# Optimization experiments

Measured on AMD Instinct MI355X. Metric: run time of the kernel, lower is better.

Reference implementation:

```python
import jax, jax.numpy as jnp
import numpy as np

S0, P0 = 4096, 64      # level0 segments, points per level0 segment
S1, P1 = 1024, 256     # level1 superpoints, points per level1 segment
C = 128                # feature dim
KNN = 3                # K (neighbor_range=1 -> 3 candidates)
N = S0 * P0


def setup_inputs() -> dict:
    key = jax.random.key(0)
    ks = jax.random.split(key, 8)
    return {
        "sp_center_feat": jax.random.normal(ks[0], (S1, C), jnp.float32),
        "sp_center_coord": jax.random.normal(ks[1], (S1, 3), jnp.float32),
        "rawPoint_feat": jax.random.normal(ks[2], (N, C), jnp.float32),
        "hilbert_feat_coord": jax.random.normal(ks[3], (N, 3), jnp.float32),
        "points_feat": jax.random.normal(ks[4], (S0, P0, C), jnp.float32),
        "points_coord": jax.random.normal(ks[5], (S0, P0, 3), jnp.float32),
        "level0_to_level1_indices": jnp.sort(jax.random.randint(ks[6], (S0,), 0, S1)).astype(jnp.int64),
        "num_segments0": S0,
        "points_per_segment0": P0,
        "num_segments1": S1,
        "points_per_segment1": P1,
        "K": KNN,
    }


def reference(sp_center_feat, sp_center_coord, rawPoint_feat, hilbert_feat_coord,
              points_feat, points_coord, level0_to_level1_indices,
              num_segments0, points_per_segment0, num_segments1, points_per_segment1, K):
    # --- neighbor superpoint candidates (neighbor_range = 1) ---
    offsets = jnp.arange(-1, 2)                                        # [3]
    nb = jnp.clip(jnp.arange(num_segments0)[:, None] + offsets[None, :], 0, num_segments0 - 1)  # [S0,3]
    sp_idx = level0_to_level1_indices[nb]                              # [S0,3]
    nb_feat = sp_center_feat[sp_idx]                                   # [S0,3,C]
    nb_coord = sp_center_coord[sp_idx]                                 # [S0,3,3]

    # --- cdist + topk (smallest K) ---
    diff = points_coord[:, :, None, :] - nb_coord[:, None, :, :]       # [S0,P0,3,3]
    dist = jnp.sqrt(jnp.maximum(jnp.sum(diff * diff, axis=-1), 0.0))   # [S0,P0,3]
    _, knn_idx = jax.lax.top_k(-dist, K)                               # [S0,P0,K], ascending distance

    # --- gather neighbor feats, dot-product similarity, softmax, argmax ---
    b = jnp.arange(num_segments0)[:, None, None]
    knn_sp_feats = nb_feat[b, knn_idx]                                 # [S0,P0,K,C]
    sim = jnp.einsum('spc,spkc->spk', points_feat, knn_sp_feats)       # [S0,P0,K]
    sim = jax.nn.softmax(sim, axis=-1)
    max_idx = jnp.argmax(sim, axis=-1)                                 # [S0,P0]

    # --- map winning neighbor slot -> superpoint id ---
    sp_knn = sp_idx[b, knn_idx]                                        # [S0,P0,K]
    assigned = jnp.take_along_axis(sp_knn, max_idx[..., None], axis=2)[..., 0]  # [S0,P0]
    point_assignments = assigned.reshape(-1)                           # [N]

    # cross_attention_update_sp is empty -> sp_center_feat passes through unchanged

    # --- scatter-mean: new superpoint centers ---
    seg_sum = jax.ops.segment_sum(hilbert_feat_coord, point_assignments, num_segments=num_segments1)
    counts = jax.ops.segment_sum(jnp.ones((point_assignments.shape[0],), hilbert_feat_coord.dtype),
                                 point_assignments, num_segments=num_segments1)
    new_sp_center_coord = seg_sum / jnp.maximum(counts, 1.0)[:, None]  # [S1,3]

    feat_dim = rawPoint_feat.shape[-1]
    hilbert_feat_level1 = rawPoint_feat.reshape(num_segments1, points_per_segment1, feat_dim)
    points_feat_out = rawPoint_feat.reshape(num_segments0, points_per_segment0, feat_dim)

    return (point_assignments, sp_center_feat, new_sp_center_coord, points_feat_out, hilbert_feat_level1)
```

## Files before the change

kernel.cpp:

```cpp
#include <hip/hip_runtime.h>

#define S0 4096
#define P0 64
#define S1 1024
#define P1 256
#define C  128
#define N_PTS (S0 * P0)

__global__ __launch_bounds__(256) void assign_kernel(
    const float* __restrict__ sp_feat,
    const float* __restrict__ pts_feat,
    const float* __restrict__ hilb,
    const int*   __restrict__ l01,
    float* __restrict__ out_assign,
    float* __restrict__ ws_sum,
    float* __restrict__ ws_cnt)
{
    __shared__ float cf[3][C];
    __shared__ float lsum[3][3];
    __shared__ float lcnt[3];
    __shared__ int   lidx[3];

    const int s    = blockIdx.x;
    const int tid  = threadIdx.x;
    const int wave = tid >> 6;
    const int lane = tid & 63;

    if (tid == 0) {
        int sm = (s - 1 < 0) ? 0 : s - 1;
        int sp = (s + 1 >= S0) ? S0 - 1 : s + 1;
        lidx[0] = l01[sm];
        lidx[1] = l01[s];
        lidx[2] = l01[sp];
    }
    if (tid < 9) lsum[tid / 3][tid % 3] = 0.0f;
    if (tid < 3) lcnt[tid] = 0.0f;
    __syncthreads();

    for (int i = tid; i < 3 * C; i += 256) {
        int k = i / C, c = i % C;
        cf[k][c] = sp_feat[(size_t)lidx[k] * C + c];
    }
    __syncthreads();

    const float* base = pts_feat + (size_t)s * P0 * C;
    const int c0 = lane * 2;

    for (int p = wave * 16; p < wave * 16 + 16; ++p) {
        float2 pf = *reinterpret_cast<const float2*>(base + p * C + c0);
        float d0 = pf.x * cf[0][c0] + pf.y * cf[0][c0 + 1];
        float d1 = pf.x * cf[1][c0] + pf.y * cf[1][c0 + 1];
        float d2 = pf.x * cf[2][c0] + pf.y * cf[2][c0 + 1];
        #pragma unroll
        for (int off = 32; off > 0; off >>= 1) {
            d0 += __shfl_xor(d0, off);
            d1 += __shfl_xor(d1, off);
            d2 += __shfl_xor(d2, off);
        }
        int kb = 0; float best = d0;
        if (d1 > best) { best = d1; kb = 1; }
        if (d2 > best) { best = d2; kb = 2; }

        const int flat = s * P0 + p;
        if (lane == 0) out_assign[flat] = (float)lidx[kb];
        if (lane < 3)  atomicAdd(&lsum[kb][lane], hilb[(size_t)flat * 3 + lane]);
        if (lane == 0) atomicAdd(&lcnt[kb], 1.0f);
    }
    __syncthreads();

    if (tid < 3) {
        atomicAdd(&ws_cnt[lidx[tid]], lcnt[tid]);
        #pragma unroll
        for (int c = 0; c < 3; ++c)
            atomicAdd(&ws_sum[(size_t)lidx[tid] * 3 + c], lsum[tid][c]);
    }
}

__global__ void finalize_kernel(const float* __restrict__ ws_sum,
                                const float* __restrict__ ws_cnt,
                                float* __restrict__ out_coord)
{
    int i = blockIdx.x * blockDim.x + threadIdx.x;
    if (i >= S1 * 3) return;
    int sp = i / 3;
    out_coord[i] = ws_sum[i] / fmaxf(ws_cnt[sp], 1.0f);
}

__global__ void copy_kernel(const float4* __restrict__ raw,
                            float4* __restrict__ o_pf,
                            float4* __restrict__ o_h1,
                            const float4* __restrict__ spf,
                            float4* __restrict__ o_spf)
{
    const long NR = (long)N_PTS * C / 4;
    const long NS = (long)S1 * C / 4;
    for (long i = (long)blockIdx.x * blockDim.x + threadIdx.x;
         i < NR; i += (long)gridDim.x * blockDim.x) {
        float4 v = raw[i];
        o_pf[i] = v;
        o_h1[i] = v;
        if (i < NS) o_spf[i] = spf[i];
    }
}

extern "C" void kernel_launch(void* const* d_in, const int* in_sizes, int n_in,
                              void* d_out, int out_size, void* d_ws, size_t ws_size,
                              hipStream_t stream) {
    const float* sp_feat  = (const float*)d_in[0];
    const float* raw      = (const float*)d_in[2];
    const float* hilb     = (const float*)d_in[3];
    const float* pts_feat = (const float*)d_in[4];
    const int*   l01      = (const int*)d_in[6];

    float* out        = (float*)d_out;
    float* out_assign = out;
    float* out_spfeat = out_assign + N_PTS;
    float* out_coord  = out_spfeat + (size_t)S1 * C;
    float* out_pf     = out_coord + (size_t)S1 * 3;
    float* out_h1     = out_pf + (size_t)S0 * P0 * C;

    float* ws_sum = (float*)d_ws;
    float* ws_cnt = ws_sum + (size_t)S1 * 3;

    hipMemsetAsync(d_ws, 0, (size_t)(S1 * 3 + S1) * sizeof(float), stream);

    assign_kernel<<<S0, 256, 0, stream>>>(sp_feat, pts_feat, hilb, l01,
                                          out_assign, ws_sum, ws_cnt);
    finalize_kernel<<<(S1 * 3 + 255) / 256, 256, 0, stream>>>(ws_sum, ws_cnt, out_coord);
    copy_kernel<<<2048, 256, 0, stream>>>(
        (const float4*)raw, (float4*)out_pf, (float4*)out_h1,
        (const float4*)sp_feat, (float4*)out_spfeat);
}
```

Before: 154.4 us.

## Process four segments per block with LDS-staged point tiles, fuse finalize into copy

The assignment kernel now handles four level-0 segments (256 points) per block, with one thread per point. Point features are staged through padded LDS in 32-channel chunks, and each thread computes its three dot products serially, replacing the per-point wave shuffle reductions. The block-local accumulators cover six neighbour slots, and global atomics are skipped for empty slots. The separate finalize kernel is folded into the copy kernel to save a launch, at the cost of extra syncs and LDS traffic in the assign kernel.

```diff
diff --git a/kernel.cpp b/kernel.cpp
--- a/kernel.cpp
+++ b/kernel.cpp
@@ -6,6 +6,11 @@
 #define P1 256
 #define C  128
 #define N_PTS (S0 * P0)
+
+#define SEG_PER_BLK 4
+#define PT_PER_BLK  256
+#define CHUNK       32
+#define PSTRIDE     36
 
 __global__ __launch_bounds__(256) void assign_kernel(
     const float* __restrict__ sp_feat,
@@ -16,86 +21,101 @@
     float* __restrict__ ws_sum,
     float* __restrict__ ws_cnt)
 {
-    __shared__ float cf[3][C];
-    __shared__ float lsum[3][3];
-    __shared__ float lcnt[3];
-    __shared__ int   lidx[3];
+    __shared__ float pt_lds[PT_PER_BLK * PSTRIDE];
+    __shared__ float cf_lds[6 * C];
+    __shared__ float lsum[6][3];
+    __shared__ float lcnt[6];
+    __shared__ int   lidx[6];
 
-    const int s    = blockIdx.x;
-    const int tid  = threadIdx.x;
-    const int wave = tid >> 6;
-    const int lane = tid & 63;
+    const int tid    = threadIdx.x;
+    const int blk    = blockIdx.x;
+    const int s_base = blk * SEG_PER_BLK;
 
-    if (tid == 0) {
-        int sm = (s - 1 < 0) ? 0 : s - 1;
-        int sp = (s + 1 >= S0) ? S0 - 1 : s + 1;
-        lidx[0] = l01[sm];
-        lidx[1] = l01[s];
-        lidx[2] = l01[sp];
+    if (tid < 6) {
+        int nb = s_base - 1 + tid;
+        nb = nb < 0 ? 0 : (nb >= S0 ? S0 - 1 : nb);
+        lidx[tid] = l01[nb];
+        lcnt[tid] = 0.0f;
     }
-    if (tid < 9) lsum[tid / 3][tid % 3] = 0.0f;
-    if (tid < 3) lcnt[tid] = 0.0f;
+    if (tid < 18) lsum[tid / 3][tid % 3] = 0.0f;
     __syncthreads();
 
-    for (int i = tid; i < 3 * C; i += 256) {
-        int k = i / C, c = i % C;
-        cf[k][c] = sp_feat[(size_t)lidx[k] * C + c];
+    for (int i = tid; i < 6 * C; i += 256)
+        cf_lds[i] = sp_feat[(size_t)lidx[i >> 7] * C + (i & (C - 1))];
+
+    const size_t blk_base = (size_t)blk * PT_PER_BLK * C;
+    const int    si       = tid >> 6;
+    float d0 = 0.f, d1 = 0.f, d2 = 0.f;
+
+    for (int ch = 0; ch < C; ch += CHUNK) {
+        #pragma unroll
+        for (int it = 0; it < 8; ++it) {
+            int i  = tid + it * 256;
+            int pt = i >> 3, q = i & 7;
+            float4 v = *reinterpret_cast<const float4*>(
+                pts_feat + blk_base + (size_t)pt * C + ch + q * 4);
+            *reinterpret_cast<float4*>(&pt_lds[pt * PSTRIDE + q * 4]) = v;
+        }
+        __syncthreads();
+
+        const float* prow = &pt_lds[tid * PSTRIDE];
+        const float* c0   = &cf_lds[(si + 0) * C + ch];
+        const float* c1   = &cf_lds[(si + 1) * C + ch];
+        const float* c2   = &cf_lds[(si + 2) * C + ch];
+        #pragma unroll
+        for (int j = 0; j < CHUNK; j += 4) {
+            float4 v  = *reinterpret_cast<const float4*>(prow + j);
+            float4 a0 = *reinterpret_cast<const float4*>(c0 + j);
+            float4 a1 = *reinterpret_cast<const float4*>(c1 + j);
+            float4 a2 = *reinterpret_cast<const float4*>(c2 + j);
+            d0 += v.x * a0.x + v.y * a0.y + v.z * a0.z + v.w * a0.w;
+            d1 += v.x * a1.x + v.y * a1.y + v.z * a1.z + v.w * a1.w;
+            d2 += v.x * a2.x + v.y * a2.y + v.z * a2.z + v.w * a2.w;
+        }
+        __syncthreads();
     }
+
+    int kb = 0; float best = d0;
+    if (d1 > best) { best = d1; kb = 1; }
+    if (d2 > best) { best = d2; kb = 2; }
+    const int slot = si + kb;
+    const int gpt  = blk * PT_PER_BLK + tid;
+
+    out_assign[gpt] = (float)lidx[slot];
+
+    const float hx = hilb[(size_t)gpt * 3 + 0];
+    const float hy = hilb[(size_t)gpt * 3 + 1];
+    const float hz = hilb[(size_t)gpt * 3 + 2];
+    atomicAdd(&lsum[slot][0], hx);
+    atomicAdd(&lsum[slot][1], hy);
+    atomicAdd(&lsum[slot][2], hz);
+    atomicAdd(&lcnt[slot], 1.0f);
     __syncthreads();
 
-    const float* base = pts_feat + (size_t)s * P0 * C;
-    const int c0 = lane * 2;
-
-    for (int p = wave * 16; p < wave * 16 + 16; ++p) {
-        float2 pf = *reinterpret_cast<const float2*>(base + p * C + c0);
-        float d0 = pf.x * cf[0][c0] + pf.y * cf[0][c0 + 1];
-        float d1 = pf.x * cf[1][c0] + pf.y * cf[1][c0 + 1];
-        float d2 = pf.x * cf[2][c0] + pf.y * cf[2][c0 + 1];
-        #pragma unroll
-        for (int off = 32; off > 0; off >>= 1) {
-            d0 += __shfl_xor(d0, off);
-            d1 += __shfl_xor(d1, off);
-            d2 += __shfl_xor(d2, off);
-        }
-        int kb = 0; float best = d0;
-        if (d1 > best) { best = d1; kb = 1; }
-        if (d2 > best) { best = d2; kb = 2; }
-
-        const int flat = s * P0 + p;
-        if (lane == 0) out_assign[flat] = (float)lidx[kb];
-        if (lane < 3)  atomicAdd(&lsum[kb][lane], hilb[(size_t)flat * 3 + lane]);
-        if (lane == 0) atomicAdd(&lcnt[kb], 1.0f);
+    if (tid < 6 && lcnt[tid] > 0.0f) {
+        atomicAdd(&ws_cnt[lidx[tid]], lcnt[tid]);
+        atomicAdd(&ws_sum[(size_t)lidx[tid] * 3 + 0], lsum[tid][0]);
+        atomicAdd(&ws_sum[(size_t)lidx[tid] * 3 + 1], lsum[tid][1]);
+        atomicAdd(&ws_sum[(size_t)lidx[tid] * 3 + 2], lsum[tid][2]);
     }
-    __syncthreads();
-
-    if (tid < 3) {
-        atomicAdd(&ws_cnt[lidx[tid]], lcnt[tid]);
-        #pragma unroll
-        for (int c = 0; c < 3; ++c)
-            atomicAdd(&ws_sum[(size_t)lidx[tid] * 3 + c], lsum[tid][c]);
-    }
-}
-
-__global__ void finalize_kernel(const float* __restrict__ ws_sum,
-                                const float* __restrict__ ws_cnt,
-                                float* __restrict__ out_coord)
-{
-    int i = blockIdx.x * blockDim.x + threadIdx.x;
-    if (i >= S1 * 3) return;
-    int sp = i / 3;
-    out_coord[i] = ws_sum[i] / fmaxf(ws_cnt[sp], 1.0f);
 }
 
 __global__ void copy_kernel(const float4* __restrict__ raw,
                             float4* __restrict__ o_pf,
                             float4* __restrict__ o_h1,
                             const float4* __restrict__ spf,
-                            float4* __restrict__ o_spf)
+                            float4* __restrict__ o_spf,
+                            const float* __restrict__ ws_sum,
+                            const float* __restrict__ ws_cnt,
+                            float* __restrict__ out_coord)
 {
+    const long gid = (long)blockIdx.x * blockDim.x + threadIdx.x;
+    if (gid < S1 * 3)
+        out_coord[gid] = ws_sum[gid] / fmaxf(ws_cnt[gid / 3], 1.0f);
+
     const long NR = (long)N_PTS * C / 4;
     const long NS = (long)S1 * C / 4;
-    for (long i = (long)blockIdx.x * blockDim.x + threadIdx.x;
-         i < NR; i += (long)gridDim.x * blockDim.x) {
+    for (long i = gid; i < NR; i += (long)gridDim.x * blockDim.x) {
         float4 v = raw[i];
         o_pf[i] = v;
         o_h1[i] = v;
@@ -124,10 +144,11 @@
 
     hipMemsetAsync(d_ws, 0, (size_t)(S1 * 3 + S1) * sizeof(float), stream);
 
-    assign_kernel<<<S0, 256, 0, stream>>>(sp_feat, pts_feat, hilb, l01,
-                                          out_assign, ws_sum, ws_cnt);
-    finalize_kernel<<<(S1 * 3 + 255) / 256, 256, 0, stream>>>(ws_sum, ws_cnt, out_coord);
+    assign_kernel<<<S0 / SEG_PER_BLK, 256, 0, stream>>>(
+        sp_feat, pts_feat, hilb, l01, out_assign, ws_sum, ws_cnt);
+
     copy_kernel<<<2048, 256, 0, stream>>>(
         (const float4*)raw, (float4*)out_pf, (float4*)out_h1,
-        (const float4*)sp_feat, (float4*)out_spfeat);
+        (const float4*)sp_feat, (float4*)out_spfeat,
+        ws_sum, ws_cnt, out_coord);
 }
```

Result: faster. 128.9 us (-16.5%).
